# Kernel optimization log

Measured on AMD Instinct MI355X. Metric: run time of the kernel, lower is better.

The kernel has to match this reference:

```python
import jax, jax.numpy as jnp
import numpy as np

NUM_EMBEDDINGS = 512
EMBEDDING_DIM = 64
COMMITMENT_COST = 0.25


def setup_inputs() -> dict:
    key = jax.random.key(0)
    k1, k2 = jax.random.split(key)
    inputs = jax.random.normal(k1, (32, EMBEDDING_DIM, 64, 64), dtype=jnp.float32)  # NCHW
    lim = 1.0 / NUM_EMBEDDINGS
    weight = jax.random.uniform(k2, (NUM_EMBEDDINGS, EMBEDDING_DIM), dtype=jnp.float32,
                                minval=-lim, maxval=lim)
    return {"inputs": inputs, "weight": weight}


def reference(inputs, weight):
    # NCHW -> NHWC, flatten to [N, D]
    x = jnp.transpose(inputs, (0, 2, 3, 1))  # [B,H,W,D]
    input_shape = x.shape
    flat = x.reshape(-1, EMBEDDING_DIM)  # [N,D]

    distances = (jnp.sum(flat ** 2, axis=1, keepdims=True)
                 + jnp.sum(weight ** 2, axis=1)
                 - 2.0 * flat @ weight.T)  # [N,K]
    encoding_indices = jnp.argmin(distances, axis=1)  # [N]
    encodings = jax.nn.one_hot(encoding_indices, NUM_EMBEDDINGS, dtype=jnp.float32)  # [N,K]

    # gather (equivalent to encodings @ weight)
    quantized = weight[encoding_indices].reshape(input_shape)  # [B,H,W,D]

    e_latent_loss = jnp.mean((jax.lax.stop_gradient(quantized) - x) ** 2)
    q_latent_loss = jnp.mean((quantized - jax.lax.stop_gradient(x)) ** 2)
    loss = q_latent_loss + COMMITMENT_COST * e_latent_loss

    # straight-through estimator
    quantized_st = x + jax.lax.stop_gradient(quantized - x)

    avg_probs = jnp.mean(encodings, axis=0)  # [K]
    perplexity = jnp.exp(-jnp.sum(avg_probs * jnp.log(avg_probs + 1e-10)))

    out = jnp.transpose(quantized_st, (0, 3, 1, 2))  # back to NCHW
    return (loss, out, perplexity, encodings)
```

## Files before the change

kernel.cpp:

```cpp
#include <hip/hip_runtime.h>

typedef short   bf16x8 __attribute__((ext_vector_type(8)));
typedef float   f32x4  __attribute__((ext_vector_type(4)));
typedef float   f32x2  __attribute__((ext_vector_type(2)));

#define NVEC   131072
#define HW     4096
#define CHW    262144
#define QOFF   1
#define PERPOFF 8388609
#define ENCOFF  8388610


__device__ inline unsigned short f2bf(float f) {
    unsigned int u = __float_as_uint(f);
    u += 0x7fffu + ((u >> 16) & 1u);
    return (unsigned short)(u >> 16);
}

__global__ __launch_bounds__(64) void vq_prep(const float* __restrict__ wt,
                                              float* __restrict__ bias,
                                              unsigned short* __restrict__ wbf,
                                              int* __restrict__ counts,
                                              double* __restrict__ loss) {
    int c = blockIdx.x, d = threadIdx.x;
    if (c == 0) {
#pragma unroll
        for (int i = 0; i < 8; ++i) counts[d * 8 + i] = 0;
        if (d == 0) loss[0] = 0.0;
    }
    float v = wt[c * 64 + d];
    wbf[c * 64 + d] = f2bf(v);
    float s = v * v;
    for (int off = 32; off; off >>= 1) s += __shfl_down(s, off, 64);
    if (d == 0) bias[c] = -0.5f * s;
}

__global__ __launch_bounds__(512, 4) void vq_assign(
    const float* __restrict__ x, const float* __restrict__ wt,
    const float* __restrict__ bias, const unsigned short* __restrict__ wbf,
    float* __restrict__ out, int* __restrict__ idx,
    int* __restrict__ counts, double* __restrict__ loss_acc)
{
    __shared__ unsigned short wl[512 * 64];
    __shared__ float  biasl[512];
    __shared__ int    hc[512];
    __shared__ int    winners[256];
    __shared__ double lred[8];

    const int t = threadIdx.x, b = blockIdx.x;
    const int batch  = b >> 4;
    const int posblk = (b & 15) << 8;

    {
        const ulonglong2* src = (const ulonglong2*)wbf;
#pragma unroll
        for (int i = 0; i < 8; ++i) {
            int u  = t + 512 * i;
            int c  = u >> 3;
            int bo = (u & 7) << 4;
            ulonglong2 v = src[u];
            *(ulonglong2*)((char*)wl + ((c << 7) | (bo ^ ((c & 7) << 4)))) = v;
        }
        biasl[t] = bias[t];
        hc[t] = 0;
    }
    __syncthreads();

    const int wv = t >> 6, l = t & 63;
    const int g  = l >> 4, cl = l & 15;
    const int posw = posblk + (wv << 5);
    const int d0 = g << 3;

    float xs[2][16];
    const float* xb = x + (size_t)batch * CHW + posw + cl;
#pragma unroll
    for (int s = 0; s < 2; ++s)
#pragma unroll
        for (int j = 0; j < 8; ++j) {
            xs[s][j]     = xb[(size_t)(d0 + j) * HW + 16 * s];
            xs[s][j + 8] = xb[(size_t)(32 + d0 + j) * HW + 16 * s];
        }

    bf16x8 af[2][2];
#pragma unroll
    for (int s = 0; s < 2; ++s)
#pragma unroll
        for (int h = 0; h < 2; ++h)
#pragma unroll
            for (int i = 0; i < 8; ++i)
                af[s][h][i] = (short)f2bf(xs[s][8 * h + i]);

    float best[2][4]; int bidx[2][4];
#pragma unroll
    for (int s = 0; s < 2; ++s)
#pragma unroll
        for (int i = 0; i < 4; ++i) { best[s][i] = -1e30f; bidx[s][i] = 0; }

    const char* wlb = (const char*)wl;
#pragma unroll 4
    for (int tt = 0; tt < 32; ++tt) {
        int c  = (tt << 4) + cl;
        int rb = c << 7;
        int sw = (c & 7) << 4;
        bf16x8 b0 = *(const bf16x8*)(wlb + (rb | ((16 * g) ^ sw)));
        bf16x8 b1 = *(const bf16x8*)(wlb + (rb | ((64 + 16 * g) ^ sw)));
        float bs = biasl[c];
#pragma unroll
        for (int s = 0; s < 2; ++s) {
            f32x4 acc = {bs, bs, bs, bs};
            acc = __builtin_amdgcn_mfma_f32_16x16x32_bf16(af[s][0], b0, acc, 0, 0, 0);
            acc = __builtin_amdgcn_mfma_f32_16x16x32_bf16(af[s][1], b1, acc, 0, 0, 0);
#pragma unroll
            for (int i = 0; i < 4; ++i)
                if (acc[i] > best[s][i]) { best[s][i] = acc[i]; bidx[s][i] = c; }
        }
    }

#pragma unroll
    for (int s = 0; s < 2; ++s)
#pragma unroll
        for (int i = 0; i < 4; ++i) {
            float bd = best[s][i]; int bi = bidx[s][i];
#pragma unroll
            for (int off = 1; off < 16; off <<= 1) {
                float od = __shfl_xor(bd, off, 64);
                int   oi = __shfl_xor(bi, off, 64);
                if (od > bd || (od == bd && oi < bi)) { bd = od; bi = oi; }
            }
            bidx[s][i] = bi;
        }

    if (cl == 0) {
#pragma unroll
        for (int s = 0; s < 2; ++s)
#pragma unroll
            for (int i = 0; i < 4; ++i) {
                int w = bidx[s][i];
                winners[(wv << 5) + (s << 4) + (g << 2) + i] = w;
                atomicAdd(&hc[w], 1);
            }
    }
    __syncthreads();

    float* outb = out + QOFF + (size_t)batch * CHW + posw + cl;
    float ls = 0.f;
#pragma unroll
    for (int s = 0; s < 2; ++s) {
        int widx = winners[(wv << 5) + (s << 4) + cl];
        float q[16];
        *(float4*)&q[0]  = *(const float4*)(wt + widx * 64 + d0);
        *(float4*)&q[4]  = *(const float4*)(wt + widx * 64 + d0 + 4);
        *(float4*)&q[8]  = *(const float4*)(wt + widx * 64 + 32 + d0);
        *(float4*)&q[12] = *(const float4*)(wt + widx * 64 + 32 + d0 + 4);
#pragma unroll
        for (int j = 0; j < 8; ++j) {
            float da = q[j]     - xs[s][j];
            float db = q[j + 8] - xs[s][j + 8];
            ls += da * da + db * db;
            outb[(size_t)(d0 + j) * HW + 16 * s]      = xs[s][j]     + da;
            outb[(size_t)(32 + d0 + j) * HW + 16 * s] = xs[s][j + 8] + db;
        }
    }

    if (t < 256)
        idx[(size_t)batch * 4096 + posblk + t] = winners[t];

    double lsd = (double)ls;
    for (int off = 32; off; off >>= 1) lsd += __shfl_down(lsd, off, 64);
    if (l == 0) lred[wv] = lsd;
    __syncthreads();
    if (t == 0) {
        double s = 0.0;
#pragma unroll
        for (int i = 0; i < 8; ++i) s += lred[i];
        atomicAdd(loss_acc, s);
    }

    int v0 = hc[t];
    if (v0) atomicAdd(&counts[t], v0);
}

__global__ __launch_bounds__(256) void vq_enc(const int* __restrict__ idx,
                                              f32x2* __restrict__ enc) {
    int gid = blockIdx.x * 256 + threadIdx.x;
    int row = gid >> 8;
    int pos = (gid & 255) << 1;
    int id = idx[row];
    f32x2 v;
    v.x = (id == pos)     ? 1.f : 0.f;
    v.y = (id == pos + 1) ? 1.f : 0.f;
    __builtin_nontemporal_store(v, &enc[gid]);
}

__global__ __launch_bounds__(512) void vq_fin(const int* __restrict__ counts,
                                              const double* __restrict__ loss_acc,
                                              float* __restrict__ out) {
    __shared__ double red[512];
    int k = threadIdx.x;
    double p = (double)counts[k] * (1.0 / 131072.0);
    red[k] = p * log(p + 1e-10);
    __syncthreads();
    for (int s = 256; s; s >>= 1) {
        if (k < s) red[k] += red[k + s];
        __syncthreads();
    }
    if (k == 0) {
        out[PERPOFF] = (float)exp(-red[0]);
        out[0] = (float)(loss_acc[0] * 1.25 / 8388608.0);
    }
}

extern "C" void kernel_launch(void* const* d_in, const int* in_sizes, int n_in,
                              void* d_out, int out_size, void* d_ws, size_t ws_size,
                              hipStream_t stream) {
    const float* x  = (const float*)d_in[0];
    const float* wt = (const float*)d_in[1];
    float* out = (float*)d_out;
    char* ws = (char*)d_ws;

    int*            counts = (int*)ws;
    double*         loss   = (double*)(ws + 2048);
    float*          bias   = (float*)(ws + 4096);
    unsigned short* wbf    = (unsigned short*)(ws + 8192);
    int*            idx    = (int*)(ws + 73728);
    float*          enc    = out + ENCOFF;

    vq_prep<<<512, 64, 0, stream>>>(wt, bias, wbf, counts, loss);
    vq_assign<<<512, 512, 0, stream>>>(x, wt, bias, wbf, out, idx, counts, loss);
    vq_enc<<<131072, 256, 0, stream>>>(idx, (f32x2*)enc);
    vq_fin<<<1, 512, 0, stream>>>(counts, loss, out);
}
```

Baseline: 98.50 us.

## Stage quantized output through LDS for coalesced stores and prefetch codebook into registers

```diff
diff --git a/kernel.cpp b/kernel.cpp
--- a/kernel.cpp
+++ b/kernel.cpp
@@ -36,42 +36,38 @@
     if (d == 0) bias[c] = -0.5f * s;
 }
 
-__global__ __launch_bounds__(512, 4) void vq_assign(
+__global__ __launch_bounds__(512) void vq_assign(
     const float* __restrict__ x, const float* __restrict__ wt,
     const float* __restrict__ bias, const unsigned short* __restrict__ wbf,
     float* __restrict__ out, int* __restrict__ idx,
     int* __restrict__ counts, double* __restrict__ loss_acc)
 {
-    __shared__ unsigned short wl[512 * 64];
+    __shared__ ulonglong2 smem[4096];
     __shared__ float  biasl[512];
     __shared__ int    hc[512];
     __shared__ int    winners[256];
     __shared__ double lred[8];
 
+    unsigned short* wl    = (unsigned short*)smem;
+    float*          trans = (float*)smem;
+
     const int t = threadIdx.x, b = blockIdx.x;
     const int batch  = b >> 4;
     const int posblk = (b & 15) << 8;
-
-    {
-        const ulonglong2* src = (const ulonglong2*)wbf;
-#pragma unroll
-        for (int i = 0; i < 8; ++i) {
-            int u  = t + 512 * i;
-            int c  = u >> 3;
-            int bo = (u & 7) << 4;
-            ulonglong2 v = src[u];
-            *(ulonglong2*)((char*)wl + ((c << 7) | (bo ^ ((c & 7) << 4)))) = v;
-        }
-        biasl[t] = bias[t];
-        hc[t] = 0;
-    }
-    __syncthreads();
 
     const int wv = t >> 6, l = t & 63;
     const int g  = l >> 4, cl = l & 15;
     const int posw = posblk + (wv << 5);
     const int d0 = g << 3;
 
+    ulonglong2 stg[8];
+    {
+        const ulonglong2* src = (const ulonglong2*)wbf;
+#pragma unroll
+        for (int i = 0; i < 8; ++i) stg[i] = src[t + 512 * i];
+    }
+    float bsl = bias[t];
+
     float xs[2][16];
     const float* xb = x + (size_t)batch * CHW + posw + cl;
 #pragma unroll
@@ -81,6 +77,17 @@
             xs[s][j]     = xb[(size_t)(d0 + j) * HW + 16 * s];
             xs[s][j + 8] = xb[(size_t)(32 + d0 + j) * HW + 16 * s];
         }
+
+#pragma unroll
+    for (int i = 0; i < 8; ++i) {
+        int u  = t + 512 * i;
+        int c  = u >> 3;
+        int bo = (u & 7) << 4;
+        *(ulonglong2*)((char*)wl + ((c << 7) | (bo ^ ((c & 7) << 4)))) = stg[i];
+    }
+    biasl[t] = bsl;
+    hc[t] = 0;
+    __syncthreads();
 
     bf16x8 af[2][2];
 #pragma unroll
@@ -143,11 +150,20 @@
     }
     __syncthreads();
 
-    float* outb = out + QOFF + (size_t)batch * CHW + posw + cl;
+    if (t < 256)
+        idx[(size_t)batch * 4096 + posblk + t] = winners[t];
+    {
+        int v0 = hc[t];
+        if (v0) atomicAdd(&counts[t], v0);
+    }
+
     float ls = 0.f;
 #pragma unroll
     for (int s = 0; s < 2; ++s) {
-        int widx = winners[(wv << 5) + (s << 4) + cl];
+        int r  = (wv << 5) + (s << 4) + cl;
+        int rb = r << 6;
+        int m  = r & 31;
+        int widx = winners[r];
         float q[16];
         *(float4*)&q[0]  = *(const float4*)(wt + widx * 64 + d0);
         *(float4*)&q[4]  = *(const float4*)(wt + widx * 64 + d0 + 4);
@@ -158,13 +174,11 @@
             float da = q[j]     - xs[s][j];
             float db = q[j + 8] - xs[s][j + 8];
             ls += da * da + db * db;
-            outb[(size_t)(d0 + j) * HW + 16 * s]      = xs[s][j]     + da;
-            outb[(size_t)(32 + d0 + j) * HW + 16 * s] = xs[s][j + 8] + db;
-        }
-    }
-
-    if (t < 256)
-        idx[(size_t)batch * 4096 + posblk + t] = winners[t];
+            int d1 = d0 + j, d2 = 32 + d0 + j;
+            trans[rb + (d1 ^ m)] = xs[s][j]     + da;
+            trans[rb + (d2 ^ m)] = xs[s][j + 8] + db;
+        }
+    }
 
     double lsd = (double)ls;
     for (int off = 32; off; off >>= 1) lsd += __shfl_down(lsd, off, 64);
@@ -177,8 +191,18 @@
         atomicAdd(loss_acc, s);
     }
 
-    int v0 = hc[t];
-    if (v0) atomicAdd(&counts[t], v0);
+    {
+        float* outp = out + QOFF + (size_t)batch * CHW + posblk;
+#pragma unroll
+        for (int dd = 0; dd < 8; ++dd) {
+            int d = (wv << 3) + dd;
+#pragma unroll
+            for (int q4 = 0; q4 < 4; ++q4) {
+                int pos = (q4 << 6) + l;
+                outp[(size_t)d * HW + pos] = trans[(pos << 6) + (d ^ (pos & 31))];
+            }
+        }
+    }
 }
 
 __global__ __launch_bounds__(256) void vq_enc(const int* __restrict__ idx,
```

Result: no change. 97.60 us (-0.9%).

## Widen one-hot encoding stores to aligned 16-byte and fold finalize into encoder

Applied to the files above, without the earlier changes.

```diff
diff --git a/kernel.cpp b/kernel.cpp
--- a/kernel.cpp
+++ b/kernel.cpp
@@ -2,7 +2,6 @@
 
 typedef short   bf16x8 __attribute__((ext_vector_type(8)));
 typedef float   f32x4  __attribute__((ext_vector_type(4)));
-typedef float   f32x2  __attribute__((ext_vector_type(2)));
 
 #define NVEC   131072
 #define HW     4096
@@ -182,32 +181,50 @@
 }
 
 __global__ __launch_bounds__(256) void vq_enc(const int* __restrict__ idx,
-                                              f32x2* __restrict__ enc) {
-    int gid = blockIdx.x * 256 + threadIdx.x;
-    int row = gid >> 8;
-    int pos = (gid & 255) << 1;
-    int id = idx[row];
-    f32x2 v;
-    v.x = (id == pos)     ? 1.f : 0.f;
-    v.y = (id == pos + 1) ? 1.f : 0.f;
-    __builtin_nontemporal_store(v, &enc[gid]);
-}
-
-__global__ __launch_bounds__(512) void vq_fin(const int* __restrict__ counts,
+                                              float* __restrict__ enc,
+                                              const int* __restrict__ counts,
                                               const double* __restrict__ loss_acc,
                                               float* __restrict__ out) {
-    __shared__ double red[512];
-    int k = threadIdx.x;
-    double p = (double)counts[k] * (1.0 / 131072.0);
-    red[k] = p * log(p + 1e-10);
-    __syncthreads();
-    for (int s = 256; s; s >>= 1) {
-        if (k < s) red[k] += red[k + s];
+    const int t = threadIdx.x, b = blockIdx.x;
+    if (b == 0) {
+        __shared__ double red[256];
+        double p0 = (double)counts[t]       * (1.0 / 131072.0);
+        double p1 = (double)counts[t + 256] * (1.0 / 131072.0);
+        red[t] = p0 * log(p0 + 1e-10) + p1 * log(p1 + 1e-10);
         __syncthreads();
-    }
-    if (k == 0) {
-        out[PERPOFF] = (float)exp(-red[0]);
-        out[0] = (float)(loss_acc[0] * 1.25 / 8388608.0);
+        for (int s = 128; s; s >>= 1) {
+            if (t < s) red[t] += red[t + s];
+            __syncthreads();
+        }
+        if (t == 0) {
+            out[PERPOFF] = (float)exp(-red[0]);
+            out[0] = (float)(loss_acc[0] * 1.25 / 8388608.0);
+            int id0 = idx[0], idL = idx[131071];
+            enc[0] = (id0 == 0) ? 1.f : 0.f;
+            enc[1] = (id0 == 1) ? 1.f : 0.f;
+            enc[67108862] = (idL == 510) ? 1.f : 0.f;
+            enc[67108863] = (idL == 511) ? 1.f : 0.f;
+        }
+    }
+
+    const unsigned gid = (unsigned)b * 256u + (unsigned)t;
+#pragma unroll 4
+    for (int i = 0; i < 32; ++i) {
+        unsigned un = (unsigned)i * 524288u + gid;
+        if (un >= 16777215u) break;
+        unsigned e0   = 2u + 4u * un;
+        unsigned row0 = e0 >> 9;
+        unsigned row3 = (e0 + 3u) >> 9;
+        int id0 = idx[row0];
+        int id3 = idx[row3];
+        f32x4 v;
+#pragma unroll
+        for (int k = 0; k < 4; ++k) {
+            unsigned p   = e0 + (unsigned)k;
+            int      idk = ((p >> 9) == row0) ? id0 : id3;
+            v[k] = ((int)(p & 511u) == idk) ? 1.f : 0.f;
+        }
+        __builtin_nontemporal_store(v, (f32x4*)(enc + e0));
     }
 }
 
@@ -228,6 +245,5 @@
 
     vq_prep<<<512, 64, 0, stream>>>(wt, bias, wbf, counts, loss);
     vq_assign<<<512, 512, 0, stream>>>(x, wt, bias, wbf, out, idx, counts, loss);
-    vq_enc<<<131072, 256, 0, stream>>>(idx, (f32x2*)enc);
-    vq_fin<<<1, 512, 0, stream>>>(counts, loss, out);
-}
+    vq_enc<<<2048, 256, 0, stream>>>(idx, enc, counts, loss, out);
+}
```

New measurement: 107.9 us. 1.1x slower.
